# Kernel optimization log

Hardware: AMD Instinct MI355X
Metric: run time of the kernel (lower is better)

The kernel has to match this reference:

```python
import jax, jax.numpy as jnp
import numpy as np

N = 50000   # nodes per node type (users, d1 items, d2 items)
E = 800000  # edges per relation (avg degree 16)
D = 128     # feature dim (in_dim == out_dim)


def setup_inputs() -> dict:
    key = jax.random.key(0)
    ks = jax.random.split(key, 24)
    f32 = jnp.float32
    inp = {
        'feat_user_d1': jax.random.normal(ks[0], (N, D), f32),
        'feat_user_d2': jax.random.normal(ks[1], (N, D), f32),
        'feat_d1': jax.random.normal(ks[2], (N, D), f32),
        'feat_d2': jax.random.normal(ks[3], (N, D), f32),
        'W_i2u_d1': jax.random.normal(ks[4], (D, D), f32) * 0.05,
        'b_i2u_d1': jnp.zeros((D,), f32),
        'W_i2u_d2': jax.random.normal(ks[5], (D, D), f32) * 0.05,
        'b_i2u_d2': jnp.zeros((D,), f32),
        'W_u2i_d1': jax.random.normal(ks[6], (D, D), f32) * 0.05,
        'b_u2i_d1': jnp.zeros((D,), f32),
        'W_u2i_d2': jax.random.normal(ks[7], (D, D), f32) * 0.05,
        'b_u2i_d2': jnp.zeros((D,), f32),
        'src_i2u_d1': jax.random.randint(ks[8], (E,), 0, N, jnp.int32),
        'dst_i2u_d1': jax.random.randint(ks[9], (E,), 0, N, jnp.int32),
        'src_i2u_d2': jax.random.randint(ks[10], (E,), 0, N, jnp.int32),
        'dst_i2u_d2': jax.random.randint(ks[11], (E,), 0, N, jnp.int32),
        'src_u2i_d1': jax.random.randint(ks[12], (E,), 0, N, jnp.int32),
        'dst_u2i_d1': jax.random.randint(ks[13], (E,), 0, N, jnp.int32),
        'src_u2i_d2': jax.random.randint(ks[14], (E,), 0, N, jnp.int32),
        'dst_u2i_d2': jax.random.randint(ks[15], (E,), 0, N, jnp.int32),
    }
    return inp


def graph_conv(x, src, dst, n_src, n_dst, W, b):
    """DGL GraphConv, norm='both', allow_zero_in_degree:
    out = D_dst^{-1/2} A D_src^{-1/2} x W + b (degrees clamped to >= 1)."""
    ones = jnp.ones(src.shape, x.dtype)
    deg_src = jnp.clip(jax.ops.segment_sum(ones, src, num_segments=n_src), 1.0)
    deg_dst = jnp.clip(jax.ops.segment_sum(ones, dst, num_segments=n_dst), 1.0)
    h = x * jax.lax.rsqrt(deg_src)[:, None]                     # [n_src, D]
    agg = jax.ops.segment_sum(h[src], dst, num_segments=n_dst)  # [n_dst, D]
    return (agg * jax.lax.rsqrt(deg_dst)[:, None]) @ W + b


def reference(feat_user_d1, feat_user_d2, feat_d1, feat_d2,
              W_i2u_d1, b_i2u_d1, W_i2u_d2, b_i2u_d2,
              W_u2i_d1, b_u2i_d1, W_u2i_d2, b_u2i_d2,
              src_i2u_d1, dst_i2u_d1, src_i2u_d2, dst_i2u_d2,
              src_u2i_d1, dst_u2i_d1, src_u2i_d2, dst_u2i_d2):
    # item -> user: each item->user conv output appended to BOTH user_d1 and
    # user_d2 lists in the torch loop, so after stack+sum both equal the sum
    # over domains.
    u1 = graph_conv(feat_d1, src_i2u_d1, dst_i2u_d1, N, N, W_i2u_d1, b_i2u_d1)
    u2 = graph_conv(feat_d2, src_i2u_d2, dst_i2u_d2, N, N, W_i2u_d2, b_i2u_d2)
    user = u1 + u2
    # user -> item: single relation per item type (stack of one, then sum).
    out_d1 = graph_conv(feat_user_d1, src_u2i_d1, dst_u2i_d1, N, N, W_u2i_d1, b_u2i_d1)
    out_d2 = graph_conv(feat_user_d2, src_u2i_d2, dst_u2i_d2, N, N, W_u2i_d2, b_u2i_d2)
    # outputs: user_d1, user_d2, d1, d2 (all [N, D]) stacked for convenience
    return jnp.stack([user, user, out_d1, out_d2], axis=0)
```

## Files before the change

kernel.cpp:

```cpp
#include <hip/hip_runtime.h>

#define N_NODES 50000
#define N_EDGES 800000
#define DIM 128
#define NBKT 256
#define BKT_NODES 196
#define BKT_MAGIC 21913099u
#define PART_CHUNK 4096
#define PART_BLOCKS ((N_EDGES + PART_CHUNK - 1) / PART_CHUNK)
#define TR2_BLOCKS ((N_NODES + 63) / 64)
#define CAP 3584

typedef int   vint4   __attribute__((ext_vector_type(4)));
typedef float vfloat4 __attribute__((ext_vector_type(4)));
typedef unsigned int vuint2 __attribute__((ext_vector_type(2)));
typedef unsigned int vuint4 __attribute__((ext_vector_type(4)));
typedef short bf16x8 __attribute__((ext_vector_type(8)));
typedef float f32x4  __attribute__((ext_vector_type(4)));

struct SrcDst4  { const int* s[4]; const int* d[4]; };
struct FeatPtrs { const float* f[4]; };
struct WPtrs    { const float* W[4]; };
struct BiasPtrs { const float* b[4]; };

__device__ inline int bkt_of(int d) { return (int)__umulhi((unsigned)d, BKT_MAGIC); }

__device__ inline unsigned f2bf(float x) {
    unsigned u = __float_as_uint(x);
    return (u + 0x7fffu + ((u >> 16) & 1u)) >> 16;
}

__global__ __launch_bounds__(256) void init(WPtrs wp, unsigned short* __restrict__ WtG,
                                            int* __restrict__ gcur) {
    if (blockIdx.x < 4) {
        __shared__ float w[64 * 129];
        const int r = blockIdx.x;
        const float* __restrict__ W = wp.W[r];
        unsigned short* o = WtG + (size_t)r * DIM * DIM;
        const int tid = threadIdx.x;

        for (int half = 0; half < 2; half++) {
            if (half) __syncthreads();
#pragma unroll
            for (int i = 0; i < 8; i++) {
                int f4 = tid + i * 256;
                int k = f4 >> 5, c4 = f4 & 31;
                float4 v = ((const float4*)W)[half * 2048 + f4];
                w[k * 129 + c4 * 4 + 0] = v.x;
                w[k * 129 + c4 * 4 + 1] = v.y;
                w[k * 129 + c4 * 4 + 2] = v.z;
                w[k * 129 + c4 * 4 + 3] = v.w;
            }
            __syncthreads();
#pragma unroll
            for (int i = 0; i < 8; i++) {
                int idx2 = tid + i * 256;
                int col = idx2 >> 4;
                int kg = half * 16 + (idx2 & 15);
                int kl = (idx2 & 15) * 4;
                vuint2 p;
                p.x = (f2bf(w[(kl + 1) * 129 + col]) << 16) | f2bf(w[(kl + 0) * 129 + col]);
                p.y = (f2bf(w[(kl + 3) * 129 + col]) << 16) | f2bf(w[(kl + 2) * 129 + col]);
                ((vuint2*)o)[col * 32 + kg] = p;
            }
        }
    } else {
        int i = (blockIdx.x - 4) * 256 + threadIdx.x;
        if (i < 2048) gcur[i] = 0;
    }
}

__global__ __launch_bounds__(256) void count_deg_fb(SrcDst4 sd, int* __restrict__ degint) {
    const int r = blockIdx.y;
    const int* __restrict__ src = sd.s[r];
    int* dg = degint + (size_t)r * N_NODES;
    int i = blockIdx.x * 256 + threadIdx.x;
    if (i < N_EDGES / 4) {
        vint4 v = __builtin_nontemporal_load((const vint4*)src + i);
        atomicAdd(&dg[v.x], 1);
        atomicAdd(&dg[v.y], 1);
        atomicAdd(&dg[v.z], 1);
        atomicAdd(&dg[v.w], 1);
    }
}

__global__ __launch_bounds__(256) void deg2rinv_fb(int* __restrict__ buf, int n) {
    int i = blockIdx.x * 256 + threadIdx.x;
    if (i < n) {
        int c = buf[i];
        ((float*)buf)[i] = rsqrtf((float)(c < 1 ? 1 : c));
    }
}

__global__ __launch_bounds__(256) void zero_fb(int* __restrict__ p, int n) {
    int i = blockIdx.x * 256 + threadIdx.x;
    if (i < n) p[i] = 0;
}

__global__ __launch_bounds__(256) void prep(
    SrcDst4 sd, int* __restrict__ gcur, int* __restrict__ gcur2,
    int* __restrict__ pairs, unsigned short* __restrict__ svals,
    FeatPtrs fp, const unsigned short* __restrict__ WtG,
    unsigned short* __restrict__ Ybase)
{
    __shared__ char smem[32768];
    const int r = blockIdx.y;
    const int tid = threadIdx.x;

    if (blockIdx.x < PART_BLOCKS) {
        int* h    = (int*)smem;
        int* lofs = h + NBKT;
        int* gb   = lofs + NBKT;
        int* cur  = gb + NBKT;
        int* wsum = cur + NBKT;
        int* stage = wsum + 8;
        unsigned char* bof = (unsigned char*)(stage + PART_CHUNK);

        const int* __restrict__ src = sd.s[r];
        const int* __restrict__ dst = sd.d[r];

        const int e0 = blockIdx.x * PART_CHUNK;
        const int n = min(PART_CHUNK, N_EDGES - e0);

        h[tid] = 0;
        __syncthreads();

        vint4 dv[4], sv[4];
#pragma unroll
        for (int c = 0; c < 4; c++) {
            if (c * 256 + tid < n / 4) {
                int i4 = e0 / 4 + c * 256 + tid;
                dv[c] = __builtin_nontemporal_load((const vint4*)dst + i4);
                sv[c] = __builtin_nontemporal_load((const vint4*)src + i4);
                atomicAdd(&h[bkt_of(dv[c].x)], 1);
                atomicAdd(&h[bkt_of(dv[c].y)], 1);
                atomicAdd(&h[bkt_of(dv[c].z)], 1);
                atomicAdd(&h[bkt_of(dv[c].w)], 1);
            }
        }
        __syncthreads();

        int hc = h[tid];
        int v = hc;
#pragma unroll
        for (int d = 1; d < 64; d <<= 1) {
            int u = __shfl_up(v, d, 64);
            if ((tid & 63) >= d) v += u;
        }
        if ((tid & 63) == 63) wsum[tid >> 6] = v;
        __syncthreads();
        int base = 0;
#pragma unroll
        for (int w2 = 0; w2 < 4; w2++)
            base += (w2 < (tid >> 6)) ? wsum[w2] : 0;
        int excl = v + base - hc;

        lofs[tid] = excl;
        cur[tid] = excl;
        gb[tid] = (r * NBKT + tid) * CAP + atomicAdd(&gcur[r * NBKT + tid], hc);
        __syncthreads();

#pragma unroll
        for (int c = 0; c < 4; c++) {
            if (c * 256 + tid < n / 4) {
#pragma unroll
                for (int j = 0; j < 4; j++) {
                    int d = (j == 0) ? dv[c].x : (j == 1) ? dv[c].y : (j == 2) ? dv[c].z : dv[c].w;
                    int s = (j == 0) ? sv[c].x : (j == 1) ? sv[c].y : (j == 2) ? sv[c].z : sv[c].w;
                    int b = bkt_of(d);
                    int dl = d - b * BKT_NODES;
                    int p = atomicAdd(&cur[b], 1);
                    stage[p] = (dl << 16) | s;
                    bof[p] = (unsigned char)b;
                }
            }
        }
        __syncthreads();

        for (int i = tid; i < n; i += 256) {
            int b = bof[i];
            __builtin_nontemporal_store(stage[i], &pairs[gb[b] + (i - lofs[b])]);
        }

        if (svals == nullptr) return;

        __syncthreads();
        h[tid] = 0;
        __syncthreads();
#pragma unroll
        for (int c = 0; c < 4; c++) {
            if (c * 256 + tid < n / 4) {
                atomicAdd(&h[bkt_of(sv[c].x)], 1);
                atomicAdd(&h[bkt_of(sv[c].y)], 1);
                atomicAdd(&h[bkt_of(sv[c].z)], 1);
                atomicAdd(&h[bkt_of(sv[c].w)], 1);
            }
        }
        __syncthreads();

        int hc2 = h[tid];
        int v2 = hc2;
#pragma unroll
        for (int d = 1; d < 64; d <<= 1) {
            int u = __shfl_up(v2, d, 64);
            if ((tid & 63) >= d) v2 += u;
        }
        if ((tid & 63) == 63) wsum[tid >> 6] = v2;
        __syncthreads();
        int base2 = 0;
#pragma unroll
        for (int w2 = 0; w2 < 4; w2++)
            base2 += (w2 < (tid >> 6)) ? wsum[w2] : 0;
        int excl2 = v2 + base2 - hc2;

        lofs[tid] = excl2;
        cur[tid] = excl2;
        gb[tid] = (r * NBKT + tid) * CAP + atomicAdd(&gcur2[r * NBKT + tid], hc2);
        __syncthreads();

#pragma unroll
        for (int c = 0; c < 4; c++) {
            if (c * 256 + tid < n / 4) {
#pragma unroll
                for (int j = 0; j < 4; j++) {
                    int s = (j == 0) ? sv[c].x : (j == 1) ? sv[c].y : (j == 2) ? sv[c].z : sv[c].w;
                    int b = bkt_of(s);
                    int sl = s - b * BKT_NODES;
                    int p = atomicAdd(&cur[b], 1);
                    stage[p] = sl;
                    bof[p] = (unsigned char)b;
                }
            }
        }
        __syncthreads();

        for (int i = tid; i < n; i += 256) {
            int b = bof[i];
            __builtin_nontemporal_store((unsigned short)stage[i],
                                        &svals[gb[b] + (i - lofs[b])]);
        }
    } else {
        unsigned short* xs = (unsigned short*)smem;
        unsigned short* Wt = (unsigned short*)(smem + 16384);

        const float* __restrict__ f = fp.f[r];
        const unsigned short* __restrict__ Wg = WtG + (size_t)r * DIM * DIM;
        unsigned short* __restrict__ Yo = Ybase + (size_t)r * N_NODES * DIM;

        const int row0 = (blockIdx.x - PART_BLOCKS) * 64;

#pragma unroll
        for (int i = 0; i < 8; i++) {
            int f4 = tid + i * 256;
            int row = f4 >> 5, c4 = f4 & 31;
            float4 v = make_float4(0.f, 0.f, 0.f, 0.f);
            if (row0 + row < N_NODES)
                v = ((const float4*)f)[(size_t)(row0 + row) * 32 + c4];
            vuint2 p;
            p.x = (f2bf(v.y) << 16) | f2bf(v.x);
            p.y = (f2bf(v.w) << 16) | f2bf(v.z);
            int byte = (row * 256 + c4 * 8) ^ ((row & 7) << 4);
            *(vuint2*)((char*)xs + byte) = p;
        }

        const int w = tid >> 6;
        const int l = tid & 63;
        const int lr = l & 15;
        const int kg = (l >> 4) * 8;

        f32x4 acc[8];
#pragma unroll
        for (int t = 0; t < 8; t++) acc[t] = (f32x4){0.f, 0.f, 0.f, 0.f};

        const int arow = w * 16 + lr;

        for (int half = 0; half < 2; half++) {
            __syncthreads();
#pragma unroll
            for (int i = 0; i < 4; i++) {
                int idx = tid + i * 256;
                int col = idx >> 3;
                int kql = idx & 7;
                vuint4 v = ((const vuint4*)Wg)[col * 16 + half * 8 + kql];
                int byte = (col * 128 + kql * 16) ^ ((col & 7) << 4);
                *(vuint4*)((char*)Wt + byte) = v;
            }
            __syncthreads();

#pragma unroll
            for (int kk = 0; kk < 2; kk++) {
                int k0 = half * 64 + kk * 32;
                int klb = kk * 32;
                bf16x8 a = *(bf16x8*)((char*)xs +
                    ((arow * 256 + (k0 + kg) * 2) ^ ((arow & 7) << 4)));
#pragma unroll
                for (int t = 0; t < 8; t++) {
                    int col = t * 16 + lr;
                    bf16x8 b = *(bf16x8*)((char*)Wt +
                        ((col * 128 + (klb + kg) * 2) ^ ((col & 7) << 4)));
                    acc[t] = __builtin_amdgcn_mfma_f32_16x16x32_bf16(a, b, acc[t], 0, 0, 0);
                }
            }
        }
        __syncthreads();

#pragma unroll
        for (int t = 0; t < 8; t++) {
#pragma unroll
            for (int rr = 0; rr < 4; rr++) {
                int row = w * 16 + (l >> 4) * 4 + rr;
                int col = t * 16 + lr;
                int byte = (row * 256 + col * 2) ^ ((row & 7) << 4);
                *(unsigned short*)((char*)xs + byte) = (unsigned short)f2bf(acc[t][rr]);
            }
        }
        __syncthreads();

#pragma unroll
        for (int i = 0; i < 4; i++) {
            int idx = tid + i * 256;
            int row = idx >> 4;
            if (row0 + row < N_NODES) {
                int byte = (row * 256 + (idx & 15) * 16) ^ ((row & 7) << 4);
                vuint4 v = *(vuint4*)((char*)xs + byte);
                __builtin_nontemporal_store(v,
                    (vuint4*)Yo + (size_t)(row0 + row) * 16 + (idx & 15));
            }
        }
    }
}

__global__ __launch_bounds__(256) void deg_kernel(
    const unsigned short* __restrict__ svals, const int* __restrict__ gcur2,
    float* __restrict__ rinv)
{
    __shared__ int cnt[BKT_NODES];
    const int r = blockIdx.y;
    const int b = blockIdx.x;
    const int tid = threadIdx.x;
    const int n = min(gcur2[r * NBKT + b], CAP);
    const unsigned short* __restrict__ sv = svals + (size_t)(r * NBKT + b) * CAP;

    if (tid < BKT_NODES) cnt[tid] = 0;
    __syncthreads();
    for (int i = tid; i < n; i += 256) atomicAdd(&cnt[sv[i]], 1);
    __syncthreads();
    const int node0 = b * BKT_NODES;
    if (tid < BKT_NODES && node0 + tid < N_NODES) {
        int c = cnt[tid];
        rinv[(size_t)r * N_NODES + node0 + tid] = rsqrtf((float)(c < 1 ? 1 : c));
    }
}

__global__ __launch_bounds__(512) void gather_sort(
    const unsigned short* __restrict__ Ybase, const int* __restrict__ pairs,
    const int* __restrict__ gcur, const float* __restrict__ rinv,
    BiasPtrs bp, float* __restrict__ out)
{
    __shared__ int h[NBKT], E[NBKT], C[NBKT], wsum[8];
    __shared__ unsigned short stage[CAP];

    const int r = blockIdx.y;
    const int b = blockIdx.x;
    const int tid = threadIdx.x;

    const int pcnt = min(gcur[r * NBKT + b], CAP);
    const int* __restrict__ pp = pairs + (size_t)(r * NBKT + b) * CAP;

    if (tid < NBKT) h[tid] = 0;
    __syncthreads();
    for (int i = tid; i < pcnt; i += 512) atomicAdd(&h[pp[i] >> 16], 1);
    __syncthreads();

    int hc = (tid < NBKT) ? h[tid] : 0;
    int v = hc;
#pragma unroll
    for (int d = 1; d < 64; d <<= 1) {
        int u = __shfl_up(v, d, 64);
        if ((tid & 63) >= d) v += u;
    }
    if (tid < NBKT && (tid & 63) == 63) wsum[tid >> 6] = v;
    __syncthreads();
    if (tid < NBKT) {
        int base = 0;
#pragma unroll
        for (int w2 = 0; w2 < 4; w2++)
            base += (w2 < (tid >> 6)) ? wsum[w2] : 0;
        int excl = v + base - hc;
        E[tid] = excl;
        C[tid] = excl;
    }
    __syncthreads();
    for (int i = tid; i < pcnt; i += 512) {
        int pk = pp[i];
        int p = atomicAdd(&C[pk >> 16], 1);
        if (p < CAP) stage[p] = (unsigned short)(pk & 0xffff);
    }
    __syncthreads();

    const int w = tid >> 6;
    const int lane = tid & 63;
    const int sub = lane >> 5;
    const int l = lane & 31;
    const int node0 = b * BKT_NODES;
    const vuint2* __restrict__ feat2 = (const vuint2*)(Ybase + (size_t)r * N_NODES * DIM);
    const float* __restrict__ rinv_src = rinv + (size_t)r * N_NODES;
    float* o_slot = out + (size_t)r * N_NODES * DIM;

    for (int nl = w; nl < BKT_NODES; nl += 8) {
        int node = node0 + nl;
        if (node >= N_NODES) break;
        const int beg = E[nl];
        const int end = C[nl];

        float a0 = 0.f, a1 = 0.f, a2 = 0.f, a3 = 0.f;
        int i = beg + sub;
        for (; i + 2 < end; i += 4) {
            int s0 = stage[i];
            int s1 = stage[i + 2];
            float sc0 = rinv_src[s0];
            float sc1 = rinv_src[s1];
            vuint2 q0 = feat2[(size_t)s0 * 32 + l];
            vuint2 q1 = feat2[(size_t)s1 * 32 + l];
            a0 = fmaf(__uint_as_float(q0.x << 16),         sc0, a0);
            a1 = fmaf(__uint_as_float(q0.x & 0xffff0000u), sc0, a1);
            a2 = fmaf(__uint_as_float(q0.y << 16),         sc0, a2);
            a3 = fmaf(__uint_as_float(q0.y & 0xffff0000u), sc0, a3);
            a0 = fmaf(__uint_as_float(q1.x << 16),         sc1, a0);
            a1 = fmaf(__uint_as_float(q1.x & 0xffff0000u), sc1, a1);
            a2 = fmaf(__uint_as_float(q1.y << 16),         sc1, a2);
            a3 = fmaf(__uint_as_float(q1.y & 0xffff0000u), sc1, a3);
        }
        if (i < end) {
            int s0 = stage[i];
            float sc0 = rinv_src[s0];
            vuint2 q0 = feat2[(size_t)s0 * 32 + l];
            a0 = fmaf(__uint_as_float(q0.x << 16),         sc0, a0);
            a1 = fmaf(__uint_as_float(q0.x & 0xffff0000u), sc0, a1);
            a2 = fmaf(__uint_as_float(q0.y << 16),         sc0, a2);
            a3 = fmaf(__uint_as_float(q0.y & 0xffff0000u), sc0, a3);
        }
        a0 += __shfl_xor(a0, 32);
        a1 += __shfl_xor(a1, 32);
        a2 += __shfl_xor(a2, 32);
        a3 += __shfl_xor(a3, 32);

        if (sub == 0) {
            int d = end - beg;
            float rd = rsqrtf((float)(d < 1 ? 1 : d));
            vfloat4 o = {a0 * rd, a1 * rd, a2 * rd, a3 * rd};
            if (r >= 2) {
                vfloat4 bv = *((const vfloat4*)bp.b[r] + l);
                o += bv;
            }
            __builtin_nontemporal_store(o, (vfloat4*)o_slot + (size_t)node * 32 + l);
        }
    }
}

__global__ __launch_bounds__(256) void combine(const float* __restrict__ b0,
                                               const float* __restrict__ b1,
                                               float* __restrict__ out) {
    const vfloat4* s0 = (const vfloat4*)out;
    const vfloat4* s1 = (const vfloat4*)(out + (size_t)N_NODES * DIM);
    const int total = N_NODES * 32;
    for (int i = blockIdx.x * 256 + threadIdx.x; i < total; i += gridDim.x * 256) {
        int c4 = i & 31;
        vfloat4 bv = *((const vfloat4*)b0 + c4) + *((const vfloat4*)b1 + c4);
        vfloat4 o = s0[i] + s1[i] + bv;
        ((vfloat4*)out)[i] = o;
        ((vfloat4*)(out + (size_t)N_NODES * DIM))[i] = o;
    }
}

extern "C" void kernel_launch(void* const* d_in, const int* in_sizes, int n_in,
                              void* d_out, int out_size, void* d_ws, size_t ws_size,
                              hipStream_t stream) {
    const float* feat_user_d1 = (const float*)d_in[0];
    const float* feat_user_d2 = (const float*)d_in[1];
    const float* feat_d1      = (const float*)d_in[2];
    const float* feat_d2      = (const float*)d_in[3];
    const float* W_i2u_d1 = (const float*)d_in[4];
    const float* b_i2u_d1 = (const float*)d_in[5];
    const float* W_i2u_d2 = (const float*)d_in[6];
    const float* b_i2u_d2 = (const float*)d_in[7];
    const float* W_u2i_d1 = (const float*)d_in[8];
    const float* b_u2i_d1 = (const float*)d_in[9];
    const float* W_u2i_d2 = (const float*)d_in[10];
    const float* b_u2i_d2 = (const float*)d_in[11];
    const int* src_i2u_d1 = (const int*)d_in[12];
    const int* dst_i2u_d1 = (const int*)d_in[13];
    const int* src_i2u_d2 = (const int*)d_in[14];
    const int* dst_i2u_d2 = (const int*)d_in[15];
    const int* src_u2i_d1 = (const int*)d_in[16];
    const int* dst_u2i_d1 = (const int*)d_in[17];
    const int* src_u2i_d2 = (const int*)d_in[18];
    const int* dst_u2i_d2 = (const int*)d_in[19];

    float* out = (float*)d_out;

    float* rinv = (float*)d_ws;
    int* gcur   = (int*)(rinv + 4 * (size_t)N_NODES);
    int* gcur2  = gcur + 4 * NBKT;
    unsigned short* WtG = (unsigned short*)(gcur2 + 4 * NBKT);
    int* pairs  = (int*)(WtG + 4 * (size_t)DIM * DIM);
    unsigned short* Y = (unsigned short*)(pairs + 4 * (size_t)NBKT * CAP);
    unsigned short* svals = Y + 4 * (size_t)N_NODES * DIM;
    size_t need_full = ((char*)(svals + 4 * (size_t)NBKT * CAP)) - (char*)d_ws;
    const bool use_svals = (ws_size >= need_full);

    WPtrs wp = {{W_i2u_d1, W_i2u_d2, W_u2i_d1, W_u2i_d2}};
    init<<<12, 256, 0, stream>>>(wp, WtG, gcur);

    SrcDst4 sd = {{src_i2u_d1, src_i2u_d2, src_u2i_d1, src_u2i_d2},
                  {dst_i2u_d1, dst_i2u_d2, dst_u2i_d1, dst_u2i_d2}};
    FeatPtrs fp = {{feat_d1, feat_d2, feat_user_d1, feat_user_d2}};

    if (!use_svals) {
        zero_fb<<<(4 * N_NODES + 255) / 256, 256, 0, stream>>>((int*)rinv, 4 * N_NODES);
        count_deg_fb<<<dim3((N_EDGES / 4 + 255) / 256, 4), 256, 0, stream>>>(sd, (int*)rinv);
        deg2rinv_fb<<<(4 * N_NODES + 255) / 256, 256, 0, stream>>>((int*)rinv, 4 * N_NODES);
    }

    prep<<<dim3(PART_BLOCKS + TR2_BLOCKS, 4), 256, 0, stream>>>(
        sd, gcur, gcur2, pairs, use_svals ? svals : nullptr, fp, WtG, Y);

    if (use_svals)
        deg_kernel<<<dim3(NBKT, 4), 256, 0, stream>>>(svals, gcur2, rinv);

    BiasPtrs bp = {{b_i2u_d1, b_i2u_d2, b_u2i_d1, b_u2i_d2}};
    gather_sort<<<dim3(NBKT, 4), 512, 0, stream>>>(Y, pairs, gcur, rinv, bp, out);

    combine<<<1024, 256, 0, stream>>>(b_i2u_d1, b_i2u_d2, out);
}
```

Before: 214.5 us.

## Fuse user-side relation sum into gather kernel and drop combine pass

The gather kernel now has the two item-to-user relations handled by the same block. Each block sorts both relations' edge buckets into separate shared staging arrays, then accumulates both contributions per user node in registers and writes the summed result with biases to both user output slots. This removes the separate combine kernel, which re-read and re-wrote two full N×D float tensors. In exchange, the user blocks each sort two relations redundantly, split the node range in halves, and use more shared memory, which may lower occupancy.

```diff
diff --git a/kernel.cpp b/kernel.cpp
--- a/kernel.cpp
+++ b/kernel.cpp
@@ -10,6 +10,7 @@
 #define PART_BLOCKS ((N_EDGES + PART_CHUNK - 1) / PART_CHUNK)
 #define TR2_BLOCKS ((N_NODES + 63) / 64)
 #define CAP 3584
+#define HALF_NODES 98
 
 typedef int   vint4   __attribute__((ext_vector_type(4)));
 typedef float vfloat4 __attribute__((ext_vector_type(4)));
@@ -357,119 +358,128 @@
     const int* __restrict__ gcur, const float* __restrict__ rinv,
     BiasPtrs bp, float* __restrict__ out)
 {
-    __shared__ int h[NBKT], E[NBKT], C[NBKT], wsum[8];
-    __shared__ unsigned short stage[CAP];
-
-    const int r = blockIdx.y;
+    __shared__ int h[NBKT], E0[NBKT], C0[NBKT], E1[NBKT], C1[NBKT], wsum[8];
+    __shared__ unsigned short stage0[CAP], stage1[CAP];
+
+    const int y = blockIdx.y;
     const int b = blockIdx.x;
     const int tid = threadIdx.x;
-
-    const int pcnt = min(gcur[r * NBKT + b], CAP);
-    const int* __restrict__ pp = pairs + (size_t)(r * NBKT + b) * CAP;
-
-    if (tid < NBKT) h[tid] = 0;
-    __syncthreads();
-    for (int i = tid; i < pcnt; i += 512) atomicAdd(&h[pp[i] >> 16], 1);
-    __syncthreads();
-
-    int hc = (tid < NBKT) ? h[tid] : 0;
-    int v = hc;
-#pragma unroll
-    for (int d = 1; d < 64; d <<= 1) {
-        int u = __shfl_up(v, d, 64);
-        if ((tid & 63) >= d) v += u;
-    }
-    if (tid < NBKT && (tid & 63) == 63) wsum[tid >> 6] = v;
-    __syncthreads();
-    if (tid < NBKT) {
-        int base = 0;
-#pragma unroll
-        for (int w2 = 0; w2 < 4; w2++)
-            base += (w2 < (tid >> 6)) ? wsum[w2] : 0;
-        int excl = v + base - hc;
-        E[tid] = excl;
-        C[tid] = excl;
-    }
-    __syncthreads();
-    for (int i = tid; i < pcnt; i += 512) {
-        int pk = pp[i];
-        int p = atomicAdd(&C[pk >> 16], 1);
-        if (p < CAP) stage[p] = (unsigned short)(pk & 0xffff);
-    }
-    __syncthreads();
+    const bool user = (y < 2);
+    const int rlo = user ? 0 : y;
+    const int nrel = user ? 2 : 1;
+
+    for (int q = 0; q < nrel; q++) {
+        int r = rlo + q;
+        unsigned short* S = q ? stage1 : stage0;
+        int* E = q ? E1 : E0;
+        int* C = q ? C1 : C0;
+        const int pcnt = min(gcur[r * NBKT + b], CAP);
+        const int* __restrict__ pp = pairs + (size_t)(r * NBKT + b) * CAP;
+
+        if (tid < NBKT) h[tid] = 0;
+        __syncthreads();
+        for (int i = tid; i < pcnt; i += 512) atomicAdd(&h[pp[i] >> 16], 1);
+        __syncthreads();
+
+        int hc = (tid < NBKT) ? h[tid] : 0;
+        int v = hc;
+#pragma unroll
+        for (int d = 1; d < 64; d <<= 1) {
+            int u = __shfl_up(v, d, 64);
+            if ((tid & 63) >= d) v += u;
+        }
+        if (tid < NBKT && (tid & 63) == 63) wsum[tid >> 6] = v;
+        __syncthreads();
+        if (tid < NBKT) {
+            int base = 0;
+#pragma unroll
+            for (int w2 = 0; w2 < 4; w2++)
+                base += (w2 < (tid >> 6)) ? wsum[w2] : 0;
+            int excl = v + base - hc;
+            E[tid] = excl;
+            C[tid] = excl;
+        }
+        __syncthreads();
+        for (int i = tid; i < pcnt; i += 512) {
+            int pk = pp[i];
+            int p = atomicAdd(&C[pk >> 16], 1);
+            if (p < CAP) S[p] = (unsigned short)(pk & 0xffff);
+        }
+        __syncthreads();
+    }
 
     const int w = tid >> 6;
     const int lane = tid & 63;
     const int sub = lane >> 5;
     const int l = lane & 31;
     const int node0 = b * BKT_NODES;
-    const vuint2* __restrict__ feat2 = (const vuint2*)(Ybase + (size_t)r * N_NODES * DIM);
-    const float* __restrict__ rinv_src = rinv + (size_t)r * N_NODES;
-    float* o_slot = out + (size_t)r * N_NODES * DIM;
-
-    for (int nl = w; nl < BKT_NODES; nl += 8) {
+    const int nlo = user ? y * HALF_NODES : 0;
+    const int nhi = user ? (y + 1) * HALF_NODES : BKT_NODES;
+
+    for (int nl = nlo + w; nl < nhi; nl += 8) {
         int node = node0 + nl;
         if (node >= N_NODES) break;
-        const int beg = E[nl];
-        const int end = C[nl];
-
-        float a0 = 0.f, a1 = 0.f, a2 = 0.f, a3 = 0.f;
-        int i = beg + sub;
-        for (; i + 2 < end; i += 4) {
-            int s0 = stage[i];
-            int s1 = stage[i + 2];
-            float sc0 = rinv_src[s0];
-            float sc1 = rinv_src[s1];
-            vuint2 q0 = feat2[(size_t)s0 * 32 + l];
-            vuint2 q1 = feat2[(size_t)s1 * 32 + l];
-            a0 = fmaf(__uint_as_float(q0.x << 16),         sc0, a0);
-            a1 = fmaf(__uint_as_float(q0.x & 0xffff0000u), sc0, a1);
-            a2 = fmaf(__uint_as_float(q0.y << 16),         sc0, a2);
-            a3 = fmaf(__uint_as_float(q0.y & 0xffff0000u), sc0, a3);
-            a0 = fmaf(__uint_as_float(q1.x << 16),         sc1, a0);
-            a1 = fmaf(__uint_as_float(q1.x & 0xffff0000u), sc1, a1);
-            a2 = fmaf(__uint_as_float(q1.y << 16),         sc1, a2);
-            a3 = fmaf(__uint_as_float(q1.y & 0xffff0000u), sc1, a3);
-        }
-        if (i < end) {
-            int s0 = stage[i];
-            float sc0 = rinv_src[s0];
-            vuint2 q0 = feat2[(size_t)s0 * 32 + l];
-            a0 = fmaf(__uint_as_float(q0.x << 16),         sc0, a0);
-            a1 = fmaf(__uint_as_float(q0.x & 0xffff0000u), sc0, a1);
-            a2 = fmaf(__uint_as_float(q0.y << 16),         sc0, a2);
-            a3 = fmaf(__uint_as_float(q0.y & 0xffff0000u), sc0, a3);
-        }
-        a0 += __shfl_xor(a0, 32);
-        a1 += __shfl_xor(a1, 32);
-        a2 += __shfl_xor(a2, 32);
-        a3 += __shfl_xor(a3, 32);
-
-        if (sub == 0) {
+
+        float t0 = 0.f, t1 = 0.f, t2 = 0.f, t3 = 0.f;
+        for (int q = 0; q < nrel; q++) {
+            int r = rlo + q;
+            const unsigned short* S = q ? stage1 : stage0;
+            const int beg = q ? E1[nl] : E0[nl];
+            const int end = q ? C1[nl] : C0[nl];
+            const vuint2* __restrict__ feat2 =
+                (const vuint2*)(Ybase + (size_t)r * N_NODES * DIM);
+            const float* __restrict__ rinv_src = rinv + (size_t)r * N_NODES;
+
+            float a0 = 0.f, a1 = 0.f, a2 = 0.f, a3 = 0.f;
+            int i = beg + sub;
+            for (; i + 2 < end; i += 4) {
+                int s0 = S[i];
+                int s1 = S[i + 2];
+                float sc0 = rinv_src[s0];
+                float sc1 = rinv_src[s1];
+                vuint2 q0 = feat2[(size_t)s0 * 32 + l];
+                vuint2 q1 = feat2[(size_t)s1 * 32 + l];
+                a0 = fmaf(__uint_as_float(q0.x << 16),         sc0, a0);
+                a1 = fmaf(__uint_as_float(q0.x & 0xffff0000u), sc0, a1);
+                a2 = fmaf(__uint_as_float(q0.y << 16),         sc0, a2);
+                a3 = fmaf(__uint_as_float(q0.y & 0xffff0000u), sc0, a3);
+                a0 = fmaf(__uint_as_float(q1.x << 16),         sc1, a0);
+                a1 = fmaf(__uint_as_float(q1.x & 0xffff0000u), sc1, a1);
+                a2 = fmaf(__uint_as_float(q1.y << 16),         sc1, a2);
+                a3 = fmaf(__uint_as_float(q1.y & 0xffff0000u), sc1, a3);
+            }
+            if (i < end) {
+                int s0 = S[i];
+                float sc0 = rinv_src[s0];
+                vuint2 q0 = feat2[(size_t)s0 * 32 + l];
+                a0 = fmaf(__uint_as_float(q0.x << 16),         sc0, a0);
+                a1 = fmaf(__uint_as_float(q0.x & 0xffff0000u), sc0, a1);
+                a2 = fmaf(__uint_as_float(q0.y << 16),         sc0, a2);
+                a3 = fmaf(__uint_as_float(q0.y & 0xffff0000u), sc0, a3);
+            }
+            a0 += __shfl_xor(a0, 32);
+            a1 += __shfl_xor(a1, 32);
+            a2 += __shfl_xor(a2, 32);
+            a3 += __shfl_xor(a3, 32);
             int d = end - beg;
             float rd = rsqrtf((float)(d < 1 ? 1 : d));
-            vfloat4 o = {a0 * rd, a1 * rd, a2 * rd, a3 * rd};
-            if (r >= 2) {
-                vfloat4 bv = *((const vfloat4*)bp.b[r] + l);
-                o += bv;
-            }
-            __builtin_nontemporal_store(o, (vfloat4*)o_slot + (size_t)node * 32 + l);
-        }
-    }
-}
-
-__global__ __launch_bounds__(256) void combine(const float* __restrict__ b0,
-                                               const float* __restrict__ b1,
-                                               float* __restrict__ out) {
-    const vfloat4* s0 = (const vfloat4*)out;
-    const vfloat4* s1 = (const vfloat4*)(out + (size_t)N_NODES * DIM);
-    const int total = N_NODES * 32;
-    for (int i = blockIdx.x * 256 + threadIdx.x; i < total; i += gridDim.x * 256) {
-        int c4 = i & 31;
-        vfloat4 bv = *((const vfloat4*)b0 + c4) + *((const vfloat4*)b1 + c4);
-        vfloat4 o = s0[i] + s1[i] + bv;
-        ((vfloat4*)out)[i] = o;
-        ((vfloat4*)(out + (size_t)N_NODES * DIM))[i] = o;
+            t0 = fmaf(a0, rd, t0); t1 = fmaf(a1, rd, t1);
+            t2 = fmaf(a2, rd, t2); t3 = fmaf(a3, rd, t3);
+        }
+
+        if (sub == 0) {
+            vfloat4 bv = *((const vfloat4*)bp.b[rlo] + l);
+            if (user) bv += *((const vfloat4*)bp.b[1] + l);
+            vfloat4 o = {t0 + bv.x, t1 + bv.y, t2 + bv.z, t3 + bv.w};
+            if (user) {
+                __builtin_nontemporal_store(o, (vfloat4*)out + (size_t)node * 32 + l);
+                __builtin_nontemporal_store(o,
+                    (vfloat4*)(out + (size_t)N_NODES * DIM) + (size_t)node * 32 + l);
+            } else {
+                __builtin_nontemporal_store(o,
+                    (vfloat4*)(out + (size_t)y * N_NODES * DIM) + (size_t)node * 32 + l);
+            }
+        }
     }
 }
 
@@ -530,6 +540,4 @@
 
     BiasPtrs bp = {{b_i2u_d1, b_i2u_d2, b_u2i_d1, b_u2i_d2}};
     gather_sort<<<dim3(NBKT, 4), 512, 0, stream>>>(Y, pairs, gcur, rinv, bp, out);
-
-    combine<<<1024, 256, 0, stream>>>(b_i2u_d1, b_i2u_d2, out);
-}
+}
```

Result: faster. 198.5 us (-7.4%).
